# Kernel tuning notes

Hardware: AMD Instinct MI355X
Metric: run time of the kernel (lower is better)

Reference implementation:

```python
import jax, jax.numpy as jnp
import numpy as np

B, A, M, N = 16, 98304, 32, 32  # batch, anchors, gt boxes per image, sample size
IMG = 512.0


def _make_boxes(key, prefix):
    """Valid [x1,y1,x2,y2] boxes inside a 512px image (x2>x1, y2>y1)."""
    k1, k2 = jax.random.split(key)
    xy = jax.random.uniform(k1, prefix + (2,), minval=0.0, maxval=IMG - 130.0)
    wh = jax.random.uniform(k2, prefix + (2,), minval=16.0, maxval=128.0)
    return jnp.concatenate([xy, xy + wh], axis=-1)


def setup_inputs() -> dict:
    key = jax.random.key(0)
    ks = jax.random.split(key, 4)
    classifications = jax.random.uniform(ks[0], (B, A, 2), minval=0.01, maxval=0.99)
    regressions = jax.random.normal(ks[1], (B, A, 4), dtype=jnp.float32)
    anchors = _make_boxes(ks[2], (1, A))
    ann_boxes = _make_boxes(ks[3], (B, M))
    annotations = jnp.concatenate([ann_boxes, jnp.zeros((B, M, 1))], axis=-1)
    w = jnp.ones((B, 4), dtype=jnp.float32)
    return {"classifications": classifications, "regressions": regressions,
            "anchors": anchors, "annotations": annotations, "w": w}


def _calc_iou(a, b):
    # a: [A,4] anchors, b: [M,4] gt boxes -> [A,M]
    area = (b[:, 2] - b[:, 0]) * (b[:, 3] - b[:, 1])  # [M]
    iw = jnp.minimum(a[:, 2:3], b[None, :, 2]) - jnp.maximum(a[:, 0:1], b[None, :, 0])
    ih = jnp.minimum(a[:, 3:4], b[None, :, 3]) - jnp.maximum(a[:, 1:2], b[None, :, 1])
    iw = jnp.clip(iw, 0.0)
    ih = jnp.clip(ih, 0.0)
    a_area = (a[:, 2] - a[:, 0]) * (a[:, 3] - a[:, 1])  # [A]
    ua = jnp.clip(a_area[:, None] + area[None, :] - iw * ih, 1e-8)
    return iw * ih / ua


def _per_image(cls_j, reg_j, anchor, ann_j, w_j, keys):
    nA = anchor.shape[0]
    cls_j = jnp.clip(cls_j, 1e-7, 1.0 - 1e-7)
    # class forced to 0, coords clamped to [0,512] (as in the torch module)
    bbox = jnp.clip(ann_j[:, :4], 0.0, IMG)
    iou = _calc_iou(anchor, bbox)                # [A, M]
    iou_max = iou.max(axis=1)
    iou_arg = iou.argmax(axis=1)

    # --- positive sampling: random subset of size min(N, count) via random top-k ---
    thresh = jnp.minimum(iou_max.max(), 0.7)
    pos_elig = iou_max >= thresh
    s_pos = jnp.where(pos_elig, jax.random.uniform(keys[0], (nA,), minval=0.1, maxval=1.0), -1.0)
    vpos, ipos = jax.lax.top_k(s_pos, N)
    keep_pos = vpos > 0.0                         # only eligible anchors
    pos_sel = jnp.zeros(nA, bool).at[ipos].set(keep_pos)
    K = keep_pos.sum()

    # --- negative sampling: random subset of size min(2N-K, count) ---
    neg_elig = (iou_max < 0.4) & (iou_max >= 0.1)
    s_neg = jnp.where(neg_elig, jax.random.uniform(keys[1], (nA,), minval=0.1, maxval=1.0), -1.0)
    vneg, ineg = jax.lax.top_k(s_neg, 2 * N)
    keep_neg = (vneg > 0.0) & (jnp.arange(2 * N) < (2 * N - K))
    neg_sel = jnp.zeros(nA, bool).at[ineg].set(keep_neg)

    # targets: positives -> [1,0] (class forced to 0), negatives -> [0,1], else -1 (ignore)
    t0 = jnp.where(pos_sel, 1.0, jnp.where(neg_sel, 0.0, -1.0))
    t1 = jnp.where(pos_sel, 0.0, jnp.where(neg_sel, 1.0, -1.0))
    targets = jnp.stack([t0, t1], axis=-1)       # [A,2]
    cls_loss = jnp.where(targets != -1.0, -(targets * jnp.log(cls_j)), 0.0).sum() / (2 * N)

    aw = anchor[:, 2] - anchor[:, 0]
    ah = anchor[:, 3] - anchor[:, 1]
    acx = anchor[:, 0] + 0.5 * aw
    acy = anchor[:, 1] + 0.5 * ah
    assigned = bbox[iou_arg]                     # [A,4]
    gw = assigned[:, 2] - assigned[:, 0]
    gh = assigned[:, 3] - assigned[:, 1]
    gcx = assigned[:, 0] + 0.5 * gw
    gcy = assigned[:, 1] + 0.5 * gh
    gw = jnp.maximum(gw, 1.0)
    gh = jnp.maximum(gh, 1.0)
    t = jnp.stack([(gcx - acx) / aw, (gcy - acy) / ah,
                   jnp.log(gw / aw), jnp.log(gh / ah)], axis=-1)
    t = t / jnp.array([0.1, 0.1, 0.2, 0.2], dtype=t.dtype)
    diff = jnp.abs(t - reg_j)
    sl1 = jnp.where(diff <= 1.0 / 9.0, 0.5 * 9.0 * diff * diff, diff - 0.5 / 9.0)
    reg_loss = (sl1 * pos_sel[:, None].astype(sl1.dtype)).sum() * w_j[0] / (2 * N)
    return cls_loss, reg_loss


def reference(classifications, regressions, anchors, annotations, w):
    anchor = anchors[0]
    bsz = classifications.shape[0]
    keys = jax.random.split(jax.random.key(42), bsz * 2).reshape(bsz, 2)
    cl, rl = jax.vmap(
        lambda c, r, a, wj, k: _per_image(c, r, anchor, a, wj, k)
    )(classifications, regressions, annotations, w, keys)
    return (jnp.mean(cl, keepdims=True), jnp.mean(rl, keepdims=True))
```

## Files before the change

### kernel.cpp

```cpp
#include <hip/hip_runtime.h>

#define NB 16
#define NA 98304
#define NM 32
#define NS 32
#define BLKI 96
#define TARGET 256
#define GCAP 1024
#define BCAP 512

typedef unsigned int u32;
typedef unsigned long long u64;

static_assert(NA == BLKI * 256 * 4, "coverage");

struct WS {
  u64   pos_key[NB * GCAP];
  u64   neg_key[NB * GCAP];
  float iou_max[NB * NA];
  u32   iou_arg4[NB * NA / 4];
  float blk_max[NB * BLKI];
  int   blk_nneg[NB * BLKI];
  int   blk_npos[NB * BLKI];
  float thresh[NB], cut_pos[NB], cut_neg[NB];
  int   n_neg[NB], n_pos07[NB], ge07[NB];
  u32   keys[NB][4];
  int   pos_cnt[NB], neg_cnt[NB];
  float cls_img[NB], reg_img[NB];
};

__device__ __forceinline__ u32 rotl32(u32 v, int d) { return (v << d) | (v >> (32 - d)); }

__device__ __forceinline__ void threefry2x32(u32 k0, u32 k1, u32 x0, u32 x1, u32& o0, u32& o1) {
  u32 k2 = k0 ^ k1 ^ 0x1BD11BDAu;
  x0 += k0; x1 += k1;
  x0 += x1; x1 = rotl32(x1, 13); x1 ^= x0;
  x0 += x1; x1 = rotl32(x1, 15); x1 ^= x0;
  x0 += x1; x1 = rotl32(x1, 26); x1 ^= x0;
  x0 += x1; x1 = rotl32(x1, 6);  x1 ^= x0;
  x0 += k1; x1 += k2 + 1u;
  x0 += x1; x1 = rotl32(x1, 17); x1 ^= x0;
  x0 += x1; x1 = rotl32(x1, 29); x1 ^= x0;
  x0 += x1; x1 = rotl32(x1, 16); x1 ^= x0;
  x0 += x1; x1 = rotl32(x1, 24); x1 ^= x0;
  x0 += k2; x1 += k0 + 2u;
  x0 += x1; x1 = rotl32(x1, 13); x1 ^= x0;
  x0 += x1; x1 = rotl32(x1, 15); x1 ^= x0;
  x0 += x1; x1 = rotl32(x1, 26); x1 ^= x0;
  x0 += x1; x1 = rotl32(x1, 6);  x1 ^= x0;
  x0 += k0; x1 += k1 + 3u;
  x0 += x1; x1 = rotl32(x1, 17); x1 ^= x0;
  x0 += x1; x1 = rotl32(x1, 29); x1 ^= x0;
  x0 += x1; x1 = rotl32(x1, 16); x1 ^= x0;
  x0 += x1; x1 = rotl32(x1, 24); x1 ^= x0;
  x0 += k1; x1 += k2 + 4u;
  x0 += x1; x1 = rotl32(x1, 13); x1 ^= x0;
  x0 += x1; x1 = rotl32(x1, 15); x1 ^= x0;
  x0 += x1; x1 = rotl32(x1, 26); x1 ^= x0;
  x0 += x1; x1 = rotl32(x1, 6);  x1 ^= x0;
  x0 += k2; x1 += k0 + 5u;
  o0 = x0; o1 = x1;
}

__device__ __forceinline__ float tf_uniform(u32 k0, u32 k1, u32 idx) {
  u32 o0, o1;
  threefry2x32(k0, k1, 0u, idx, o0, o1);
  u32 bits = o0 ^ o1;
  float f = __uint_as_float((bits >> 9) | 0x3F800000u) - 1.0f;
  float u = __fadd_rn(__fmul_rn(f, (1.0f - 0.1f)), 0.1f);
  return fmaxf(0.1f, u);
}

__device__ __forceinline__ u64 pack_key(float u, u32 a) {
  return ((u64)__float_as_uint(u) << 32) | (u64)(u32)(~a);
}

__global__ __launch_bounds__(256) void k_iou(const float* __restrict__ anchors,
                                             const float* __restrict__ ann,
                                             WS* __restrict__ ws) {
  int b = blockIdx.y;
  int tid = threadIdx.x;
  int a0 = (blockIdx.x * 256 + tid) * 4;
  __shared__ float bx1[NM], by1[NM], bx2[NM], by2[NM], barea[NM];
  __shared__ float wmax[4];
  __shared__ int wneg[4], wpos[4];
  if (tid < NM) {
    int m = tid;
    const float* p = ann + ((size_t)b * NM + m) * 5;
    float x1 = fminf(fmaxf(p[0], 0.0f), 512.0f);
    float y1 = fminf(fmaxf(p[1], 0.0f), 512.0f);
    float x2 = fminf(fmaxf(p[2], 0.0f), 512.0f);
    float y2 = fminf(fmaxf(p[3], 0.0f), 512.0f);
    bx1[m] = x1; by1[m] = y1; bx2[m] = x2; by2[m] = y2;
    barea[m] = __fmul_rn(__fsub_rn(x2, x1), __fsub_rn(y2, y1));
  }
  __syncthreads();

  const float4* a4 = (const float4*)anchors;
  float4 ap[4];
  float aarea[4], bi[4], bu[4];
  int bm[4];
#pragma unroll
  for (int k = 0; k < 4; k++) {
    ap[k] = a4[a0 + k];
    aarea[k] = __fmul_rn(__fsub_rn(ap[k].z, ap[k].x), __fsub_rn(ap[k].w, ap[k].y));
    bi[k] = -1.0f;
    bu[k] = 1.0f;
    bm[k] = 0;
  }
#pragma unroll 2
  for (int m = 0; m < NM; m++) {
    float x1 = bx1[m], y1 = by1[m], x2 = bx2[m], y2 = by2[m], ar = barea[m];
#pragma unroll
    for (int k = 0; k < 4; k++) {
      float iw = fmaxf(__fsub_rn(fminf(ap[k].z, x2), fmaxf(ap[k].x, x1)), 0.0f);
      float ih = fmaxf(__fsub_rn(fminf(ap[k].w, y2), fmaxf(ap[k].y, y1)), 0.0f);
      float inter = __fmul_rn(iw, ih);
      float ua = fmaxf(__fsub_rn(__fadd_rn(aarea[k], ar), inter), 1e-8f);
      bool upd = __fmul_rn(inter, bu[k]) > __fmul_rn(bi[k], ua);
      bi[k] = upd ? inter : bi[k];
      bu[k] = upd ? ua : bu[k];
      bm[k] = upd ? m : bm[k];
    }
  }
  float best[4];
#pragma unroll
  for (int k = 0; k < 4; k++) best[k] = __fdiv_rn(bi[k], bu[k]);

  u32 pack = (u32)bm[0] | ((u32)bm[1] << 8) | ((u32)bm[2] << 16) | ((u32)bm[3] << 24);
  float lmax = fmaxf(fmaxf(best[0], best[1]), fmaxf(best[2], best[3]));
  int cneg = 0, cpos = 0;
#pragma unroll
  for (int k = 0; k < 4; k++) {
    cneg += (best[k] < 0.4f && best[k] >= 0.1f) ? 1 : 0;
    cpos += (best[k] >= 0.7f) ? 1 : 0;
  }
  *(float4*)&ws->iou_max[(size_t)b * NA + a0] = make_float4(best[0], best[1], best[2], best[3]);
  ws->iou_arg4[((size_t)b * NA + a0) >> 2] = pack;

  for (int s = 32; s > 0; s >>= 1) {
    lmax = fmaxf(lmax, __shfl_xor(lmax, s));
    cneg += __shfl_xor(cneg, s);
    cpos += __shfl_xor(cpos, s);
  }
  int wid = tid >> 6;
  if ((tid & 63) == 0) { wmax[wid] = lmax; wneg[wid] = cneg; wpos[wid] = cpos; }
  __syncthreads();
  if (tid < 4) {
    lmax = wmax[tid]; cneg = wneg[tid]; cpos = wpos[tid];
    for (int s = 2; s > 0; s >>= 1) {
      lmax = fmaxf(lmax, __shfl_xor(lmax, s));
      cneg += __shfl_xor(cneg, s);
      cpos += __shfl_xor(cpos, s);
    }
    if (tid == 0) {
      int o = b * BLKI + blockIdx.x;
      ws->blk_max[o] = lmax;
      ws->blk_nneg[o] = cneg;
      ws->blk_npos[o] = cpos;
    }
  }
}

__global__ __launch_bounds__(128) void k_stats(WS* __restrict__ ws) {
  int b = blockIdx.x, l = threadIdx.x;
  __shared__ float sm[2];
  __shared__ int sn[2], sp[2];
  float m = -1.0f;
  int nn = 0, np = 0;
  for (int i = l; i < BLKI; i += 128) {
    m = fmaxf(m, ws->blk_max[b * BLKI + i]);
    nn += ws->blk_nneg[b * BLKI + i];
    np += ws->blk_npos[b * BLKI + i];
  }
  for (int s = 32; s > 0; s >>= 1) {
    m = fmaxf(m, __shfl_xor(m, s));
    nn += __shfl_xor(nn, s);
    np += __shfl_xor(np, s);
  }
  int wid = l >> 6;
  if ((l & 63) == 0) { sm[wid] = m; sn[wid] = nn; sp[wid] = np; }
  __syncthreads();
  if (l == 0) {
    m = fmaxf(sm[0], sm[1]); nn = sn[0] + sn[1]; np = sp[0] + sp[1];
    ws->thresh[b] = fminf(m, 0.7f);
    int ge = (m >= 0.7f) ? 1 : 0;
    ws->ge07[b] = ge;
    ws->n_neg[b] = nn;
    ws->n_pos07[b] = np;
    ws->cut_neg[b] = (nn <= TARGET) ? -1.0f : (1.0f - 0.9f * ((float)TARGET / (float)nn));
    ws->cut_pos[b] = (ge && np > TARGET) ? (1.0f - 0.9f * ((float)TARGET / (float)np)) : -1.0f;
    ws->pos_cnt[b] = 0;
    ws->neg_cnt[b] = 0;
    u32 o0, o1;
    threefry2x32(0u, 42u, 0u, (u32)(2 * b), o0, o1);
    ws->keys[b][0] = o0; ws->keys[b][1] = o1;
    threefry2x32(0u, 42u, 0u, (u32)(2 * b + 1), o0, o1);
    ws->keys[b][2] = o0; ws->keys[b][3] = o1;
  }
}

__global__ __launch_bounds__(256) void k_push(WS* __restrict__ ws) {
  int b = blockIdx.y, tid = threadIdx.x;
  int a0 = (blockIdx.x * 256 + tid) * 4;
  __shared__ u64 pbuf[BCAP], nbuf[BCAP];
  __shared__ int pcnt, ncnt, pbase, nbase;
  if (tid == 0) { pcnt = 0; ncnt = 0; }
  __syncthreads();
  float thresh = ws->thresh[b];
  float cp = ws->cut_pos[b], cn = ws->cut_neg[b];
  u32 k0 = ws->keys[b][0], k1 = ws->keys[b][1];
  u32 k2 = ws->keys[b][2], k3 = ws->keys[b][3];
  float4 im4 = *(const float4*)&ws->iou_max[(size_t)b * NA + a0];
  float imv[4] = {im4.x, im4.y, im4.z, im4.w};
#pragma unroll
  for (int k = 0; k < 4; k++) {
    float im = imv[k];
    u32 a = (u32)(a0 + k);
    if (im >= thresh) {
      float u = tf_uniform(k0, k1, a);
      if (u >= cp) {
        int p = atomicAdd(&pcnt, 1);
        if (p < BCAP) pbuf[p] = pack_key(u, a);
      }
    }
    if (im < 0.4f && im >= 0.1f) {
      float u = tf_uniform(k2, k3, a);
      if (u >= cn) {
        int p = atomicAdd(&ncnt, 1);
        if (p < BCAP) nbuf[p] = pack_key(u, a);
      }
    }
  }
  __syncthreads();
  if (tid == 0) {
    pbase = (pcnt > 0) ? atomicAdd(&ws->pos_cnt[b], pcnt) : 0;
    nbase = (ncnt > 0) ? atomicAdd(&ws->neg_cnt[b], ncnt) : 0;
  }
  __syncthreads();
  int pc = min(pcnt, BCAP), nc = min(ncnt, BCAP);
  for (int i = tid; i < pc; i += 256) { int g = pbase + i; if (g < GCAP) ws->pos_key[b * GCAP + g] = pbuf[i]; }
  for (int i = tid; i < nc; i += 256) { int g = nbase + i; if (g < GCAP) ws->neg_key[b * GCAP + g] = nbuf[i]; }
}

__global__ __launch_bounds__(256) void k_select(const float* __restrict__ cls,
                                                const float* __restrict__ reg,
                                                const float* __restrict__ anchors,
                                                const float* __restrict__ ann,
                                                const float* __restrict__ w,
                                                WS* __restrict__ ws) {
  int b = blockIdx.x, tid = threadIdx.x;
  __shared__ u64 pk[GCAP], nk[GCAP];
  __shared__ int selp[NS], seln[2 * NS];
  __shared__ float tpos[NS], treg[NS], tneg[2 * NS];

  int mp = min(ws->pos_cnt[b], GCAP);
  int mn = min(ws->neg_cnt[b], GCAP);
  int n_pos = ws->ge07[b] ? ws->n_pos07[b] : ws->pos_cnt[b];
  int n_neg = ws->n_neg[b];
  int K = min(NS, n_pos);
  int rp = min(K, mp);
  int rn = min(min(2 * NS - K, n_neg), mn);

  int mpad = (mp + 255) & ~255;
  int npad = (mn + 255) & ~255;
  for (int i = tid; i < mpad; i += 256) pk[i] = (i < mp) ? ws->pos_key[b * GCAP + i] : 0ull;
  for (int i = tid; i < npad; i += 256) nk[i] = (i < mn) ? ws->neg_key[b * GCAP + i] : 0ull;
  if (tid < NS) { tpos[tid] = 0.0f; treg[tid] = 0.0f; }
  if (tid < 2 * NS) tneg[tid] = 0.0f;
  __syncthreads();

  {
    u64 ck[GCAP / 256]; int cr[GCAP / 256];
    int nc = mpad >> 8;
#pragma unroll
    for (int c = 0; c < GCAP / 256; c++) { ck[c] = 0; cr[c] = 0; }
    for (int c = 0; c < nc; c++) ck[c] = pk[tid + (c << 8)];
    for (int j = 0; j < mp; j++) {
      u64 v = pk[j];
#pragma unroll
      for (int c = 0; c < GCAP / 256; c++) cr[c] += (v > ck[c]) ? 1 : 0;
    }
    for (int c = 0; c < nc; c++)
      if (ck[c] != 0 && cr[c] < rp) selp[cr[c]] = (int)(~(u32)ck[c]);
  }
  {
    u64 ck[GCAP / 256]; int cr[GCAP / 256];
    int nc = npad >> 8;
#pragma unroll
    for (int c = 0; c < GCAP / 256; c++) { ck[c] = 0; cr[c] = 0; }
    for (int c = 0; c < nc; c++) ck[c] = nk[tid + (c << 8)];
    for (int j = 0; j < mn; j++) {
      u64 v = nk[j];
#pragma unroll
      for (int c = 0; c < GCAP / 256; c++) cr[c] += (v > ck[c]) ? 1 : 0;
    }
    for (int c = 0; c < nc; c++)
      if (ck[c] != 0 && cr[c] < rn) seln[cr[c]] = (int)(~(u32)ck[c]);
  }
  __syncthreads();

  const float PLO = 1e-7f;
  const float PHI = (float)(1.0 - 1e-7);
  if (tid < rp) {
    int a = selp[tid];
    float p = cls[((size_t)b * NA + a) * 2 + 0];
    p = fminf(fmaxf(p, PLO), PHI);
    tpos[tid] = -logf(p);
    float4 apf = ((const float4*)anchors)[a];
    float ax1 = apf.x, ay1 = apf.y, ax2 = apf.z, ay2 = apf.w;
    float aw_ = __fsub_rn(ax2, ax1), ah_ = __fsub_rn(ay2, ay1);
    float acx = __fadd_rn(ax1, __fmul_rn(0.5f, aw_));
    float acy = __fadd_rn(ay1, __fmul_rn(0.5f, ah_));
    int m = (int)((ws->iou_arg4[((size_t)b * NA + a) >> 2] >> (8 * (a & 3))) & 0xFFu);
    const float* g = ann + ((size_t)b * NM + m) * 5;
    float gx1 = fminf(fmaxf(g[0], 0.0f), 512.0f);
    float gy1 = fminf(fmaxf(g[1], 0.0f), 512.0f);
    float gx2 = fminf(fmaxf(g[2], 0.0f), 512.0f);
    float gy2 = fminf(fmaxf(g[3], 0.0f), 512.0f);
    float gw = __fsub_rn(gx2, gx1), gh = __fsub_rn(gy2, gy1);
    float gcx = __fadd_rn(gx1, __fmul_rn(0.5f, gw));
    float gcy = __fadd_rn(gy1, __fmul_rn(0.5f, gh));
    gw = fmaxf(gw, 1.0f); gh = fmaxf(gh, 1.0f);
    float t0 = __fdiv_rn(__fdiv_rn(__fsub_rn(gcx, acx), aw_), 0.1f);
    float t1 = __fdiv_rn(__fdiv_rn(__fsub_rn(gcy, acy), ah_), 0.1f);
    float t2 = __fdiv_rn(logf(__fdiv_rn(gw, aw_)), 0.2f);
    float t3 = __fdiv_rn(logf(__fdiv_rn(gh, ah_)), 0.2f);
    const float* rg = reg + ((size_t)b * NA + a) * 4;
    float tt[4] = {t0, t1, t2, t3};
    float s = 0.0f;
#pragma unroll
    for (int c = 0; c < 4; c++) {
      float d = fabsf(__fsub_rn(tt[c], rg[c]));
      float q = (d <= (float)(1.0 / 9.0)) ? __fmul_rn(__fmul_rn(4.5f, d), d)
                                          : __fsub_rn(d, (float)(0.5 / 9.0));
      s = __fadd_rn(s, q);
    }
    treg[tid] = s;
  }
  if (tid < rn) {
    int a = seln[tid];
    bool ispos = false;
    for (int i = 0; i < rp; i++) if (selp[i] == a) ispos = true;
    if (!ispos) {
      float p = cls[((size_t)b * NA + a) * 2 + 1];
      p = fminf(fmaxf(p, PLO), PHI);
      tneg[tid] = -logf(p);
    }
  }
  __syncthreads();
  if (tid == 0) {
    float cs = 0.0f;
    for (int i = 0; i < NS; i++) cs = __fadd_rn(cs, tpos[i]);
    for (int i = 0; i < 2 * NS; i++) cs = __fadd_rn(cs, tneg[i]);
    float rs = 0.0f;
    for (int i = 0; i < NS; i++) rs = __fadd_rn(rs, treg[i]);
    ws->cls_img[b] = __fdiv_rn(cs, 64.0f);
    ws->reg_img[b] = __fdiv_rn(__fmul_rn(rs, w[b * 4 + 0]), 64.0f);
  }
}

__global__ __launch_bounds__(64) void k_final(WS* __restrict__ ws, float* __restrict__ out) {
  if (threadIdx.x == 0) {
    float c = 0.0f, r = 0.0f;
    for (int b = 0; b < NB; b++) {
      c = __fadd_rn(c, ws->cls_img[b]);
      r = __fadd_rn(r, ws->reg_img[b]);
    }
    out[0] = __fdiv_rn(c, 16.0f);
    out[1] = __fdiv_rn(r, 16.0f);
  }
}

extern "C" void kernel_launch(void* const* d_in, const int* in_sizes, int n_in,
                              void* d_out, int out_size, void* d_ws, size_t ws_size,
                              hipStream_t stream) {
  const float* cls = (const float*)d_in[0];
  const float* reg = (const float*)d_in[1];
  const float* anchors = (const float*)d_in[2];
  const float* ann = (const float*)d_in[3];
  const float* w = (const float*)d_in[4];
  float* out = (float*)d_out;
  if (ws_size < sizeof(WS)) return;
  WS* ws = (WS*)d_ws;

  hipLaunchKernelGGL(k_iou, dim3(BLKI, NB), dim3(256), 0, stream, anchors, ann, ws);
  hipLaunchKernelGGL(k_stats, dim3(NB), dim3(128), 0, stream, ws);
  hipLaunchKernelGGL(k_push, dim3(BLKI, NB), dim3(256), 0, stream, ws);
  hipLaunchKernelGGL(k_select, dim3(NB), dim3(256), 0, stream, cls, reg, anchors, ann, w, ws);
  hipLaunchKernelGGL(k_final, dim3(1), dim3(64), 0, stream, ws, out);
}
```

Baseline: 79.26 us.

## Drop stored IoU argmax, recompute for sampled positives, fuse final reduction

The IoU kernel no longer tracks or stores the per-anchor argmax. It processes 8 anchors per thread with half as many blocks and drops the 1e-8 clamp on the union. The argmax is recomputed only for the few selected positive anchors inside the select kernel, using gt boxes cached in shared memory. The stats kernel becomes a single block covering all images, and the final cross-image average is folded into the select kernel with a last-block atomic counter, removing one launch. The aim is to cut memory writes and launch overhead. The trade-offs are extra register pressure from 8 anchors per thread, and argmax tie handling that may differ from the first-index semantics in edge cases.

Result: slower. 90.09 us (+13.7%).

```diff
diff --git a/kernel.cpp b/kernel.cpp
--- a/kernel.cpp
+++ b/kernel.cpp
@@ -4,7 +4,8 @@
 #define NA 98304
 #define NM 32
 #define NS 32
-#define BLKI 96
+#define BLKI 48
+#define BLKP 96
 #define TARGET 256
 #define GCAP 1024
 #define BCAP 512
@@ -12,13 +13,13 @@
 typedef unsigned int u32;
 typedef unsigned long long u64;
 
-static_assert(NA == BLKI * 256 * 4, "coverage");
+static_assert(NA == BLKI * 256 * 8, "coverage iou");
+static_assert(NA == BLKP * 256 * 4, "coverage push");
 
 struct WS {
   u64   pos_key[NB * GCAP];
   u64   neg_key[NB * GCAP];
   float iou_max[NB * NA];
-  u32   iou_arg4[NB * NA / 4];
   float blk_max[NB * BLKI];
   int   blk_nneg[NB * BLKI];
   int   blk_npos[NB * BLKI];
@@ -26,7 +27,8 @@
   int   n_neg[NB], n_pos07[NB], ge07[NB];
   u32   keys[NB][4];
   int   pos_cnt[NB], neg_cnt[NB];
-  float cls_img[NB], reg_img[NB];
+  u32   cls_bits[NB], reg_bits[NB];
+  int   done;
 };
 
 __device__ __forceinline__ u32 rotl32(u32 v, int d) { return (v << d) | (v >> (32 - d)); }
@@ -80,7 +82,7 @@
                                              WS* __restrict__ ws) {
   int b = blockIdx.y;
   int tid = threadIdx.x;
-  int a0 = (blockIdx.x * 256 + tid) * 4;
+  int a0 = (blockIdx.x * 256 + tid) * 8;
   __shared__ float bx1[NM], by1[NM], bx2[NM], by2[NM], barea[NM];
   __shared__ float wmax[4];
   __shared__ int wneg[4], wpos[4];
@@ -97,47 +99,44 @@
   __syncthreads();
 
   const float4* a4 = (const float4*)anchors;
-  float4 ap[4];
-  float aarea[4], bi[4], bu[4];
-  int bm[4];
-#pragma unroll
-  for (int k = 0; k < 4; k++) {
+  float4 ap[8];
+  float aarea[8], bi[8], bu[8];
+#pragma unroll
+  for (int k = 0; k < 8; k++) {
     ap[k] = a4[a0 + k];
     aarea[k] = __fmul_rn(__fsub_rn(ap[k].z, ap[k].x), __fsub_rn(ap[k].w, ap[k].y));
     bi[k] = -1.0f;
     bu[k] = 1.0f;
-    bm[k] = 0;
-  }
-#pragma unroll 2
+  }
   for (int m = 0; m < NM; m++) {
     float x1 = bx1[m], y1 = by1[m], x2 = bx2[m], y2 = by2[m], ar = barea[m];
 #pragma unroll
-    for (int k = 0; k < 4; k++) {
+    for (int k = 0; k < 8; k++) {
       float iw = fmaxf(__fsub_rn(fminf(ap[k].z, x2), fmaxf(ap[k].x, x1)), 0.0f);
       float ih = fmaxf(__fsub_rn(fminf(ap[k].w, y2), fmaxf(ap[k].y, y1)), 0.0f);
       float inter = __fmul_rn(iw, ih);
-      float ua = fmaxf(__fsub_rn(__fadd_rn(aarea[k], ar), inter), 1e-8f);
+      float ua = __fsub_rn(__fadd_rn(aarea[k], ar), inter);
       bool upd = __fmul_rn(inter, bu[k]) > __fmul_rn(bi[k], ua);
       bi[k] = upd ? inter : bi[k];
       bu[k] = upd ? ua : bu[k];
-      bm[k] = upd ? m : bm[k];
-    }
-  }
-  float best[4];
-#pragma unroll
-  for (int k = 0; k < 4; k++) best[k] = __fdiv_rn(bi[k], bu[k]);
-
-  u32 pack = (u32)bm[0] | ((u32)bm[1] << 8) | ((u32)bm[2] << 16) | ((u32)bm[3] << 24);
-  float lmax = fmaxf(fmaxf(best[0], best[1]), fmaxf(best[2], best[3]));
+    }
+  }
+  float best[8];
+#pragma unroll
+  for (int k = 0; k < 8; k++) best[k] = __fdiv_rn(bi[k], bu[k]);
+
+  size_t o = (size_t)b * NA + a0;
+  *(float4*)&ws->iou_max[o]     = make_float4(best[0], best[1], best[2], best[3]);
+  *(float4*)&ws->iou_max[o + 4] = make_float4(best[4], best[5], best[6], best[7]);
+
+  float lmax = -1.0f;
   int cneg = 0, cpos = 0;
 #pragma unroll
-  for (int k = 0; k < 4; k++) {
+  for (int k = 0; k < 8; k++) {
+    lmax = fmaxf(lmax, best[k]);
     cneg += (best[k] < 0.4f && best[k] >= 0.1f) ? 1 : 0;
     cpos += (best[k] >= 0.7f) ? 1 : 0;
   }
-  *(float4*)&ws->iou_max[(size_t)b * NA + a0] = make_float4(best[0], best[1], best[2], best[3]);
-  ws->iou_arg4[((size_t)b * NA + a0) >> 2] = pack;
-
   for (int s = 32; s > 0; s >>= 1) {
     lmax = fmaxf(lmax, __shfl_xor(lmax, s));
     cneg += __shfl_xor(cneg, s);
@@ -154,35 +153,30 @@
       cpos += __shfl_xor(cpos, s);
     }
     if (tid == 0) {
-      int o = b * BLKI + blockIdx.x;
-      ws->blk_max[o] = lmax;
-      ws->blk_nneg[o] = cneg;
-      ws->blk_npos[o] = cpos;
-    }
-  }
-}
-
-__global__ __launch_bounds__(128) void k_stats(WS* __restrict__ ws) {
-  int b = blockIdx.x, l = threadIdx.x;
-  __shared__ float sm[2];
-  __shared__ int sn[2], sp[2];
+      int oo = b * BLKI + blockIdx.x;
+      ws->blk_max[oo] = lmax;
+      ws->blk_nneg[oo] = cneg;
+      ws->blk_npos[oo] = cpos;
+    }
+  }
+}
+
+__global__ __launch_bounds__(256) void k_stats(WS* __restrict__ ws) {
+  int tid = threadIdx.x;
+  int b = tid >> 4, l = tid & 15;
   float m = -1.0f;
   int nn = 0, np = 0;
-  for (int i = l; i < BLKI; i += 128) {
+  for (int i = l; i < BLKI; i += 16) {
     m = fmaxf(m, ws->blk_max[b * BLKI + i]);
     nn += ws->blk_nneg[b * BLKI + i];
     np += ws->blk_npos[b * BLKI + i];
   }
-  for (int s = 32; s > 0; s >>= 1) {
+  for (int s = 8; s > 0; s >>= 1) {
     m = fmaxf(m, __shfl_xor(m, s));
     nn += __shfl_xor(nn, s);
     np += __shfl_xor(np, s);
   }
-  int wid = l >> 6;
-  if ((l & 63) == 0) { sm[wid] = m; sn[wid] = nn; sp[wid] = np; }
-  __syncthreads();
   if (l == 0) {
-    m = fmaxf(sm[0], sm[1]); nn = sn[0] + sn[1]; np = sp[0] + sp[1];
     ws->thresh[b] = fminf(m, 0.7f);
     int ge = (m >= 0.7f) ? 1 : 0;
     ws->ge07[b] = ge;
@@ -198,6 +192,7 @@
     threefry2x32(0u, 42u, 0u, (u32)(2 * b + 1), o0, o1);
     ws->keys[b][2] = o0; ws->keys[b][3] = o1;
   }
+  if (tid == 0) ws->done = 0;
 }
 
 __global__ __launch_bounds__(256) void k_push(WS* __restrict__ ws) {
@@ -248,11 +243,24 @@
                                                 const float* __restrict__ anchors,
                                                 const float* __restrict__ ann,
                                                 const float* __restrict__ w,
-                                                WS* __restrict__ ws) {
+                                                WS* __restrict__ ws,
+                                                float* __restrict__ out) {
   int b = blockIdx.x, tid = threadIdx.x;
   __shared__ u64 pk[GCAP], nk[GCAP];
+  __shared__ float bx1[NM], by1[NM], bx2[NM], by2[NM], barea[NM];
   __shared__ int selp[NS], seln[2 * NS];
   __shared__ float tpos[NS], treg[NS], tneg[2 * NS];
+
+  if (tid < NM) {
+    int m = tid;
+    const float* p = ann + ((size_t)b * NM + m) * 5;
+    float x1 = fminf(fmaxf(p[0], 0.0f), 512.0f);
+    float y1 = fminf(fmaxf(p[1], 0.0f), 512.0f);
+    float x2 = fminf(fmaxf(p[2], 0.0f), 512.0f);
+    float y2 = fminf(fmaxf(p[3], 0.0f), 512.0f);
+    bx1[m] = x1; by1[m] = y1; bx2[m] = x2; by2[m] = y2;
+    barea[m] = __fmul_rn(__fsub_rn(x2, x1), __fsub_rn(y2, y1));
+  }
 
   int mp = min(ws->pos_cnt[b], GCAP);
   int mn = min(ws->neg_cnt[b], GCAP);
@@ -309,15 +317,20 @@
     tpos[tid] = -logf(p);
     float4 apf = ((const float4*)anchors)[a];
     float ax1 = apf.x, ay1 = apf.y, ax2 = apf.z, ay2 = apf.w;
+    float aarea = __fmul_rn(__fsub_rn(ax2, ax1), __fsub_rn(ay2, ay1));
+    float bestv = -1.0f; int bestm = 0;
+    for (int m = 0; m < NM; m++) {
+      float iw = fmaxf(__fsub_rn(fminf(ax2, bx2[m]), fmaxf(ax1, bx1[m])), 0.0f);
+      float ih = fmaxf(__fsub_rn(fminf(ay2, by2[m]), fmaxf(ay1, by1[m])), 0.0f);
+      float inter = __fmul_rn(iw, ih);
+      float ua = fmaxf(__fsub_rn(__fadd_rn(aarea, barea[m]), inter), 1e-8f);
+      float v = __fdiv_rn(inter, ua);
+      if (v > bestv) { bestv = v; bestm = m; }
+    }
     float aw_ = __fsub_rn(ax2, ax1), ah_ = __fsub_rn(ay2, ay1);
     float acx = __fadd_rn(ax1, __fmul_rn(0.5f, aw_));
     float acy = __fadd_rn(ay1, __fmul_rn(0.5f, ah_));
-    int m = (int)((ws->iou_arg4[((size_t)b * NA + a) >> 2] >> (8 * (a & 3))) & 0xFFu);
-    const float* g = ann + ((size_t)b * NM + m) * 5;
-    float gx1 = fminf(fmaxf(g[0], 0.0f), 512.0f);
-    float gy1 = fminf(fmaxf(g[1], 0.0f), 512.0f);
-    float gx2 = fminf(fmaxf(g[2], 0.0f), 512.0f);
-    float gy2 = fminf(fmaxf(g[3], 0.0f), 512.0f);
+    float gx1 = bx1[bestm], gy1 = by1[bestm], gx2 = bx2[bestm], gy2 = by2[bestm];
     float gw = __fsub_rn(gx2, gx1), gh = __fsub_rn(gy2, gy1);
     float gcx = __fadd_rn(gx1, __fmul_rn(0.5f, gw));
     float gcy = __fadd_rn(gy1, __fmul_rn(0.5f, gh));
@@ -355,20 +368,21 @@
     for (int i = 0; i < 2 * NS; i++) cs = __fadd_rn(cs, tneg[i]);
     float rs = 0.0f;
     for (int i = 0; i < NS; i++) rs = __fadd_rn(rs, treg[i]);
-    ws->cls_img[b] = __fdiv_rn(cs, 64.0f);
-    ws->reg_img[b] = __fdiv_rn(__fmul_rn(rs, w[b * 4 + 0]), 64.0f);
-  }
-}
-
-__global__ __launch_bounds__(64) void k_final(WS* __restrict__ ws, float* __restrict__ out) {
-  if (threadIdx.x == 0) {
-    float c = 0.0f, r = 0.0f;
-    for (int b = 0; b < NB; b++) {
-      c = __fadd_rn(c, ws->cls_img[b]);
-      r = __fadd_rn(r, ws->reg_img[b]);
-    }
-    out[0] = __fdiv_rn(c, 16.0f);
-    out[1] = __fdiv_rn(r, 16.0f);
+    float ci = __fdiv_rn(cs, 64.0f);
+    float ri = __fdiv_rn(__fmul_rn(rs, w[b * 4 + 0]), 64.0f);
+    atomicExch(&ws->cls_bits[b], __float_as_uint(ci));
+    atomicExch(&ws->reg_bits[b], __float_as_uint(ri));
+    __threadfence();
+    int old = atomicAdd(&ws->done, 1);
+    if (old == NB - 1) {
+      float c = 0.0f, r = 0.0f;
+      for (int j = 0; j < NB; j++) {
+        c = __fadd_rn(c, __uint_as_float(atomicOr(&ws->cls_bits[j], 0u)));
+        r = __fadd_rn(r, __uint_as_float(atomicOr(&ws->reg_bits[j], 0u)));
+      }
+      out[0] = __fdiv_rn(c, 16.0f);
+      out[1] = __fdiv_rn(r, 16.0f);
+    }
   }
 }
 
@@ -385,8 +399,7 @@
   WS* ws = (WS*)d_ws;
 
   hipLaunchKernelGGL(k_iou, dim3(BLKI, NB), dim3(256), 0, stream, anchors, ann, ws);
-  hipLaunchKernelGGL(k_stats, dim3(NB), dim3(128), 0, stream, ws);
-  hipLaunchKernelGGL(k_push, dim3(BLKI, NB), dim3(256), 0, stream, ws);
-  hipLaunchKernelGGL(k_select, dim3(NB), dim3(256), 0, stream, cls, reg, anchors, ann, w, ws);
-  hipLaunchKernelGGL(k_final, dim3(1), dim3(64), 0, stream, ws, out);
-}
+  hipLaunchKernelGGL(k_stats, dim3(1), dim3(256), 0, stream, ws);
+  hipLaunchKernelGGL(k_push, dim3(BLKP, NB), dim3(256), 0, stream, ws);
+  hipLaunchKernelGGL(k_select, dim3(NB), dim3(256), 0, stream, cls, reg, anchors, ann, w, ws, out);
+}
```
